# Performance work log

Measured on AMD Instinct MI355X. Metric: run time of the kernel, lower is better.

The kernel has to match this reference:

```python
import jax, jax.numpy as jnp
import numpy as np

N_NODES = 100000
N_EDGES = 1600000
D_FEAT = 128
HIDDEN = 256


def setup_inputs() -> dict:
    key = jax.random.key(0)
    k1, k2, k3, k4, k5, k6, k7 = jax.random.split(key, 7)
    h = jax.random.normal(k1, (N_NODES, D_FEAT), dtype=jnp.float32)
    src = jax.random.randint(k2, (N_EDGES,), 0, N_NODES, dtype=jnp.int64)
    dst = jax.random.randint(k3, (N_EDGES,), 0, N_NODES, dtype=jnp.int64)
    # Linear weights, torch layout: W [out, in], b [out]
    lim1 = 1.0 / np.sqrt(2 * D_FEAT)
    W1_w = jax.random.uniform(k4, (HIDDEN, 2 * D_FEAT), minval=-lim1, maxval=lim1, dtype=jnp.float32)
    W1_b = jax.random.uniform(k5, (HIDDEN,), minval=-lim1, maxval=lim1, dtype=jnp.float32)
    lim2 = 1.0 / np.sqrt(HIDDEN)
    W2_w = jax.random.uniform(k6, (1, HIDDEN), minval=-lim2, maxval=lim2, dtype=jnp.float32)
    W2_b = jax.random.uniform(k7, (1,), minval=-lim2, maxval=lim2, dtype=jnp.float32)
    return {"h": h, "src": src, "dst": dst, "W1_w": W1_w, "W1_b": W1_b, "W2_w": W2_w, "W2_b": W2_b}


def reference(h, src, dst, W1_w, W1_b, W2_w, W2_b):
    # gather per-edge src/dst node features and concat: [E, 2D]
    x = jnp.concatenate([h[src], h[dst]], axis=1)
    # Linear -> ReLU -> Linear, squeeze last dim -> [E]
    hid = jax.nn.relu(x @ W1_w.T + W1_b)          # [E, H]
    score = (hid @ W2_w.T + W2_b)[:, 0]           # [E]
    return score
```

## Files before the change

### kernel.cpp

```cpp
#include <hip/hip_runtime.h>


#define NNODES 100000
#define E_TOTAL 1600000
#define D 128
#define K2 256
#define H 256

typedef short bf16x8 __attribute__((ext_vector_type(8)));
typedef short bf16x4 __attribute__((ext_vector_type(4)));
typedef float f32x4 __attribute__((ext_vector_type(4)));
typedef const __attribute__((address_space(1))) unsigned short* gas_t;
typedef __attribute__((address_space(3))) unsigned short* las_t;

__device__ __forceinline__ unsigned short f2bf(float f) {
    unsigned u = __float_as_uint(f);
    u += 0x7fff + ((u >> 16) & 1);
    return (unsigned short)(u >> 16);
}
__device__ __forceinline__ float bf2f(unsigned short s) {
    return __uint_as_float((unsigned)s << 16);
}

__global__ void cvt_kernel(const float* __restrict__ h, const float* __restrict__ w1,
                           unsigned short* __restrict__ hbf, unsigned short* __restrict__ w1bf,
                           int n4h, int n4w) {
    int i = blockIdx.x * blockDim.x + threadIdx.x;
    const float* s; unsigned short* d; int j;
    if (i < n4h) { s = h; d = hbf; j = i; }
    else if (i < n4h + n4w) { s = w1; d = w1bf; j = i - n4h; }
    else return;
    float4 v = ((const float4*)s)[j];
    ushort4 o;
    o.x = f2bf(v.x); o.y = f2bf(v.y); o.z = f2bf(v.z); o.w = f2bf(v.w);
    ((ushort4*)d)[j] = o;
}

__global__ void cvt_w1(const float* __restrict__ W1, unsigned short* __restrict__ w1bf, int n4) {
    int i = blockIdx.x * blockDim.x + threadIdx.x;
    if (i >= n4) return;
    float4 v = ((const float4*)W1)[i];
    ushort4 o;
    o.x = f2bf(v.x); o.y = f2bf(v.y); o.z = f2bf(v.z); o.w = f2bf(v.w);
    ((ushort4*)w1bf)[i] = o;
}

__global__ __launch_bounds__(256, 2) void u_gemm2(
    const unsigned short* __restrict__ hbf,
    const unsigned short* __restrict__ w1bf,
    const float* __restrict__ b1,
    unsigned short* __restrict__ Us,
    unsigned short* __restrict__ Ud)
{
    __shared__ __align__(16) unsigned short A[64 * 128];
    __shared__ __align__(16) unsigned short S[64 * 268];

    const int tid = threadIdx.x;
    const int wave = tid >> 6;
    const int lane = tid & 63;
    const int l15 = lane & 15;
    const int quad = lane >> 4;

    const int tile = blockIdx.x >> 1;
    const int half = blockIdx.x & 1;
    const int r0 = tile * 64;
    int rows = NNODES - r0; if (rows > 64) rows = 64;
    const int koff = half * 128;
    unsigned short* U = half ? Ud : Us;

#pragma unroll
    for (int it = 0; it < 4; ++it) {
        const int s = it * 256 + tid;
        const int r = s >> 4;
        const int p = s & 15;
        const int c = p ^ (r & 15);
        if (r < rows)
            __builtin_amdgcn_global_load_lds(
                (gas_t)(hbf + (size_t)(r0 + r) * D + c * 8),
                (las_t)(A + it * 2048 + wave * 512), 16, 0, 0);
    }

    bf16x8 B[4][4];
    float bias[4];
#pragma unroll
    for (int nt = 0; nt < 4; ++nt) {
        const int n = wave * 64 + nt * 16 + l15;
        bias[nt] = half ? 0.f : b1[n];
#pragma unroll
        for (int kit = 0; kit < 4; ++kit)
            B[kit][nt] = *(const bf16x8*)(w1bf + (size_t)n * K2 + koff + kit * 32 + quad * 8);
    }

    __syncthreads();

    f32x4 acc[4][4];
    const f32x4 zero = {0.f, 0.f, 0.f, 0.f};
#pragma unroll
    for (int ms = 0; ms < 4; ++ms)
#pragma unroll
        for (int nt = 0; nt < 4; ++nt)
            acc[ms][nt] = zero;

#pragma unroll
    for (int kit = 0; kit < 4; ++kit) {
        bf16x8 a[4];
#pragma unroll
        for (int ms = 0; ms < 4; ++ms) {
            const int row = ms * 16 + l15;
            const int p = (kit * 4 + quad) ^ l15;
            a[ms] = *(const bf16x8*)&A[row * 128 + p * 8];
        }
#pragma unroll
        for (int ms = 0; ms < 4; ++ms)
#pragma unroll
            for (int nt = 0; nt < 4; ++nt)
                acc[ms][nt] = __builtin_amdgcn_mfma_f32_16x16x32_bf16(
                    a[ms], B[kit][nt], acc[ms][nt], 0, 0, 0);
    }

#pragma unroll
    for (int ms = 0; ms < 4; ++ms)
#pragma unroll
        for (int r = 0; r < 4; ++r) {
            const int m = ms * 16 + quad * 4 + r;
#pragma unroll
            for (int nt = 0; nt < 4; ++nt)
                S[m * 268 + wave * 64 + nt * 16 + l15] =
                    f2bf(acc[ms][nt][r] + bias[nt]);
        }
    __syncthreads();

#pragma unroll
    for (int i = 0; i < 8; ++i) {
        const int j = i * 256 + tid;
        const int row = j >> 5;
        const int cc = j & 31;
        if (row < rows) {
            bf16x8 vv = *(const bf16x8*)&S[row * 268 + cc * 8];
            *(bf16x8*)(U + (size_t)(r0 + row) * H + cc * 8) = vv;
        }
    }
}

__global__ __launch_bounds__(256) void edge_score(
    const unsigned short* __restrict__ Us,
    const unsigned short* __restrict__ Ud,
    const int* __restrict__ srcE,
    const int* __restrict__ dstE,
    const float* __restrict__ w2,
    const float* __restrict__ b2p,
    float* __restrict__ out,
    int grp0, int ngrp)
{
    const int gt = blockIdx.x * 256 + threadIdx.x;
    const int l = gt & 15;
    const int q = gt >> 4;
    const int Q = (gridDim.x * 256) >> 4;

    float w2v[16];
#pragma unroll
    for (int j = 0; j < 16; ++j) w2v[j] = w2[l * 16 + j];
    const float b2 = *b2p;

    for (int g = grp0 + q; g < grp0 + ngrp; g += Q) {
        const int e0 = g * 4;
        const int4 s4 = *(const int4*)(srcE + e0);
        const int4 d4 = *(const int4*)(dstE + e0);
        const int sv[4] = {s4.x, s4.y, s4.z, s4.w};
        const int dv[4] = {d4.x, d4.y, d4.z, d4.w};

        bf16x8 u[4][2], v[4][2];
#pragma unroll
        for (int k = 0; k < 4; ++k) {
            const bf16x8* us = (const bf16x8*)(Us + (size_t)sv[k] * H + l * 16);
            const bf16x8* ud = (const bf16x8*)(Ud + (size_t)dv[k] * H + l * 16);
            u[k][0] = us[0]; u[k][1] = us[1];
            v[k][0] = ud[0]; v[k][1] = ud[1];
        }

        float4 res;
        float* resp = (float*)&res;
#pragma unroll
        for (int k = 0; k < 4; ++k) {
            float acc = 0.f;
#pragma unroll
            for (int j = 0; j < 8; ++j) {
                float hv = bf2f((unsigned short)u[k][0][j]) + bf2f((unsigned short)v[k][0][j]);
                acc = fmaf(fmaxf(hv, 0.f), w2v[j], acc);
            }
#pragma unroll
            for (int j = 0; j < 8; ++j) {
                float hv = bf2f((unsigned short)u[k][1][j]) + bf2f((unsigned short)v[k][1][j]);
                acc = fmaf(fmaxf(hv, 0.f), w2v[j + 8], acc);
            }
            acc += __shfl_xor(acc, 1, 16);
            acc += __shfl_xor(acc, 2, 16);
            acc += __shfl_xor(acc, 4, 16);
            acc += __shfl_xor(acc, 8, 16);
            resp[k] = acc + b2;
        }
        if (l == 0) *(float4*)(out + e0) = res;
    }
}


#define TILE_M 32
#define NTILES (E_TOTAL / TILE_M)
#define GRID 2500

#if defined(__has_attribute)
#if __has_attribute(amdgpu_waves_per_eu)
#define LB __launch_bounds__(256) __attribute__((amdgpu_waves_per_eu(2, 2)))
#else
#define LB __launch_bounds__(256, 2)
#endif
#else
#define LB __launch_bounds__(256, 2)
#endif

__global__ LB void edge_mlp(
    const unsigned short* __restrict__ hbf,
    const int* __restrict__ srcE,
    const int* __restrict__ dstE,
    const unsigned short* __restrict__ w1bf,
    const float* __restrict__ b1,
    const float* __restrict__ w2,
    const float* __restrict__ b2p,
    float* __restrict__ out)
{
    __shared__ __align__(16) unsigned short X[2][TILE_M * K2];
    __shared__ float red[2][TILE_M][5];

    const int tid = threadIdx.x;
    const int wave = tid >> 6;
    const int lane = tid & 63;
    const int lane15 = lane & 15;
    const int quad = lane >> 4;

    bf16x8 B[8][4];
#pragma unroll
    for (int kit = 0; kit < 8; ++kit)
#pragma unroll
        for (int nt = 0; nt < 4; ++nt) {
            int n = wave * 64 + nt * 16 + lane15;
            int k = kit * 32 + quad * 8;
            B[kit][nt] = *(const bf16x8*)(w1bf + n * K2 + k);
        }

    float b1v[4], w2v[4];
#pragma unroll
    for (int nt = 0; nt < 4; ++nt) {
        int n = wave * 64 + nt * 16 + lane15;
        b1v[nt] = b1[n];
        w2v[nt] = w2[n];
    }
    const float b2 = *b2p;

    const int r_off = tid >> 5;
    const int c = (tid & 31) ^ (r_off & 7);
    const int half = c >> 4;
    const int fc = c & 15;
    const int* idx_base = half ? dstE : srcE;
    const int gshort = fc * 8;

    const int t0 = blockIdx.x;
    int inode[4];

#pragma unroll
    for (int it = 0; it < 4; ++it)
        inode[it] = idx_base[t0 * TILE_M + it * 8 + r_off];
#pragma unroll
    for (int it = 0; it < 4; ++it)
        __builtin_amdgcn_global_load_lds(
            (gas_t)(hbf + inode[it] * D + gshort),
            (las_t)(&X[0][0] + it * 2048 + wave * 512), 16, 0, 0);
    {
        const int t1 = t0 + GRID;
#pragma unroll
        for (int it = 0; it < 4; ++it)
            inode[it] = idx_base[t1 * TILE_M + it * 8 + r_off];
    }

    int buf = 0;
    int prev_eb = -1;

    for (int tile = t0; tile < NTILES; tile += GRID) {
        __syncthreads();

        const int nt1 = tile + GRID;
        if (nt1 < NTILES) {
            unsigned short* Xn = &X[buf ^ 1][0];
#pragma unroll
            for (int it = 0; it < 4; ++it)
                __builtin_amdgcn_global_load_lds(
                    (gas_t)(hbf + inode[it] * D + gshort),
                    (las_t)(Xn + it * 2048 + wave * 512), 16, 0, 0);
        }
        const int nt2 = tile + 2 * GRID;
        if (nt2 < NTILES) {
            const int eb2 = nt2 * TILE_M;
#pragma unroll
            for (int it = 0; it < 4; ++it)
                inode[it] = idx_base[eb2 + it * 8 + r_off];
        }
        if (prev_eb >= 0 && tid < TILE_M) {
            float s = b2;
#pragma unroll
            for (int w = 0; w < 4; ++w) s += red[buf ^ 1][tid][w];
            out[prev_eb + tid] = s;
        }

        const unsigned short* Xc = &X[buf][0];
        f32x4 acc[2][4];
        const f32x4 zero = {0.f, 0.f, 0.f, 0.f};
#pragma unroll
        for (int ms = 0; ms < 2; ++ms)
#pragma unroll
            for (int nt = 0; nt < 4; ++nt)
                acc[ms][nt] = zero;

#pragma unroll
        for (int kit = 0; kit < 8; ++kit) {
            const int p8 = (((kit * 4 + quad) ^ (lane15 & 7))) * 8;
            bf16x8 a[2];
#pragma unroll
            for (int ms = 0; ms < 2; ++ms)
                a[ms] = *(const bf16x8*)&Xc[(ms * 16 + lane15) * K2 + p8];
#pragma unroll
            for (int ms = 0; ms < 2; ++ms)
#pragma unroll
                for (int nt = 0; nt < 4; ++nt)
                    acc[ms][nt] = __builtin_amdgcn_mfma_f32_16x16x32_bf16(
                        a[ms], B[kit][nt], acc[ms][nt], 0, 0, 0);
        }

#pragma unroll
        for (int ms = 0; ms < 2; ++ms)
#pragma unroll
            for (int r = 0; r < 4; ++r) {
                float p = 0.f;
#pragma unroll
                for (int nt = 0; nt < 4; ++nt) {
                    float hv = acc[ms][nt][r] + b1v[nt];
                    p = fmaf(fmaxf(hv, 0.f), w2v[nt], p);
                }
                p += __shfl_xor(p, 1, 16);
                p += __shfl_xor(p, 2, 16);
                p += __shfl_xor(p, 4, 16);
                p += __shfl_xor(p, 8, 16);
                if (lane15 == 0) red[buf][ms * 16 + quad * 4 + r][wave] = p;
            }
        prev_eb = tile * TILE_M;
        buf ^= 1;
    }

    __syncthreads();
    if (prev_eb >= 0 && tid < TILE_M) {
        float s = b2;
#pragma unroll
        for (int w = 0; w < 4; ++w) s += red[buf ^ 1][tid][w];
        out[prev_eb + tid] = s;
    }
}


extern "C" void kernel_launch(void* const* d_in, const int* in_sizes, int n_in,
                              void* d_out, int out_size, void* d_ws, size_t ws_size,
                              hipStream_t stream) {
    const float* h    = (const float*)d_in[0];
    const int*   srcE = (const int*)d_in[1];
    const int*   dstE = (const int*)d_in[2];
    const float* W1   = (const float*)d_in[3];
    const float* b1   = (const float*)d_in[4];
    const float* w2   = (const float*)d_in[5];
    const float* b2   = (const float*)d_in[6];
    float* out = (float*)d_out;

    char* ws = (char*)d_ws;
    const size_t offUs   = 0;
    const size_t offUd   = 51200000;
    const size_t offHbf  = 102400000;
    const size_t offW1v2 = 128000000;
    const size_t needV2  = offW1v2 + 131072;
    const size_t offW1v1 = 102400000;
    const size_t needV1  = offW1v1 + 131072;

    const int NGRP = E_TOTAL / 4;

    if (ws_size >= needV2) {
        unsigned short* Us   = (unsigned short*)(ws + offUs);
        unsigned short* Ud   = (unsigned short*)(ws + offUd);
        unsigned short* hbf  = (unsigned short*)(ws + offHbf);
        unsigned short* w1bf = (unsigned short*)(ws + offW1v2);

        int n4h = NNODES * D / 4, n4w = H * K2 / 4;
        cvt_kernel<<<(n4h + n4w + 255) / 256, 256, 0, stream>>>(h, W1, hbf, w1bf, n4h, n4w);
        u_gemm2<<<2 * ((NNODES + 63) / 64), 256, 0, stream>>>(hbf, w1bf, b1, Us, Ud);

        const int C = NGRP / 4;
        edge_score<<<2048, 256, 0, stream>>>(Us, Ud, srcE, dstE, w2, b2, out, 0 * C, C);
        edge_score<<<2048, 256, 0, stream>>>(Us, Ud, srcE, dstE, w2, b2, out, 1 * C, C);
        edge_score<<<2048, 256, 0, stream>>>(Us, Ud, srcE, dstE, w2, b2, out, 2 * C, C);
        edge_score<<<2048, 256, 0, stream>>>(Us, Ud, srcE, dstE, w2, b2, out, 3 * C, C);
    } else if (ws_size >= needV1) {
        unsigned short* hbf  = (unsigned short*)d_ws;
        unsigned short* w1bf = hbf + (size_t)NNODES * D;
        int n4h = NNODES * D / 4, n4w = H * K2 / 4;
        cvt_kernel<<<(n4h + n4w + 255) / 256, 256, 0, stream>>>(h, W1, hbf, w1bf, n4h, n4w);
        edge_mlp<<<GRID, 256, 0, stream>>>(hbf, srcE, dstE, w1bf, b1, w2, b2, out);
    } else {
        unsigned short* hbf  = (unsigned short*)d_ws;
        unsigned short* w1bf = hbf + (size_t)NNODES * D;
        int n4h = NNODES * D / 4, n4w = H * K2 / 4;
        cvt_kernel<<<(n4h + n4w + 255) / 256, 256, 0, stream>>>(h, W1, hbf, w1bf, n4h, n4w);
        edge_mlp<<<GRID, 256, 0, stream>>>(hbf, srcE, dstE, w1bf, b1, w2, b2, out);
    }
}
```

Before: 367.9 us.

## Split node GEMM over output halves, drop LDS staging, merge edge launches

The node-level GEMM now splits each tile's 256 output columns across two blocks. This halves per-thread accumulators and B registers, and the launch bound rises to four blocks per CU. The LDS staging buffer for output is removed: each lane writes packed pairs of bf16 straight to global in an interleaved column order, and the edge kernel permutes its w2 weights to match. The four edge_score launches are merged into one larger grid, which cuts launch overhead. The trade-offs are smaller, less coalesced global stores and A tiles loaded twice.

```diff
diff --git a/kernel.cpp b/kernel.cpp
--- a/kernel.cpp
+++ b/kernel.cpp
@@ -8,7 +8,6 @@
 #define H 256
 
 typedef short bf16x8 __attribute__((ext_vector_type(8)));
-typedef short bf16x4 __attribute__((ext_vector_type(4)));
 typedef float f32x4 __attribute__((ext_vector_type(4)));
 typedef const __attribute__((address_space(1))) unsigned short* gas_t;
 typedef __attribute__((address_space(3))) unsigned short* las_t;
@@ -36,16 +35,7 @@
     ((ushort4*)d)[j] = o;
 }
 
-__global__ void cvt_w1(const float* __restrict__ W1, unsigned short* __restrict__ w1bf, int n4) {
-    int i = blockIdx.x * blockDim.x + threadIdx.x;
-    if (i >= n4) return;
-    float4 v = ((const float4*)W1)[i];
-    ushort4 o;
-    o.x = f2bf(v.x); o.y = f2bf(v.y); o.z = f2bf(v.z); o.w = f2bf(v.w);
-    ((ushort4*)w1bf)[i] = o;
-}
-
-__global__ __launch_bounds__(256, 2) void u_gemm2(
+__global__ __launch_bounds__(256, 4) void u_gemm3(
     const unsigned short* __restrict__ hbf,
     const unsigned short* __restrict__ w1bf,
     const float* __restrict__ b1,
@@ -53,7 +43,6 @@
     unsigned short* __restrict__ Ud)
 {
     __shared__ __align__(16) unsigned short A[64 * 128];
-    __shared__ __align__(16) unsigned short S[64 * 268];
 
     const int tid = threadIdx.x;
     const int wave = tid >> 6;
@@ -61,8 +50,9 @@
     const int l15 = lane & 15;
     const int quad = lane >> 4;
 
-    const int tile = blockIdx.x >> 1;
-    const int half = blockIdx.x & 1;
+    const int tile = blockIdx.x >> 2;
+    const int half = (blockIdx.x >> 1) & 1;
+    const int nh = blockIdx.x & 1;
     const int r0 = tile * 64;
     int rows = NNODES - r0; if (rows > 64) rows = 64;
     const int koff = half * 128;
@@ -80,11 +70,11 @@
                 (las_t)(A + it * 2048 + wave * 512), 16, 0, 0);
     }
 
-    bf16x8 B[4][4];
-    float bias[4];
-#pragma unroll
-    for (int nt = 0; nt < 4; ++nt) {
-        const int n = wave * 64 + nt * 16 + l15;
+    bf16x8 B[4][2];
+    float bias[2];
+#pragma unroll
+    for (int nt = 0; nt < 2; ++nt) {
+        const int n = nh * 128 + wave * 32 + nt * 16 + l15;
         bias[nt] = half ? 0.f : b1[n];
 #pragma unroll
         for (int kit = 0; kit < 4; ++kit)
@@ -93,12 +83,12 @@
 
     __syncthreads();
 
-    f32x4 acc[4][4];
+    f32x4 acc[4][2];
     const f32x4 zero = {0.f, 0.f, 0.f, 0.f};
 #pragma unroll
     for (int ms = 0; ms < 4; ++ms)
 #pragma unroll
-        for (int nt = 0; nt < 4; ++nt)
+        for (int nt = 0; nt < 2; ++nt)
             acc[ms][nt] = zero;
 
 #pragma unroll
@@ -113,31 +103,22 @@
 #pragma unroll
         for (int ms = 0; ms < 4; ++ms)
 #pragma unroll
-            for (int nt = 0; nt < 4; ++nt)
+            for (int nt = 0; nt < 2; ++nt)
                 acc[ms][nt] = __builtin_amdgcn_mfma_f32_16x16x32_bf16(
                     a[ms], B[kit][nt], acc[ms][nt], 0, 0, 0);
     }
 
-#pragma unroll
-    for (int ms = 0; ms < 4; ++ms)
+    const int coff = nh * 128 + wave * 32 + l15 * 2;
+#pragma unroll
+    for (int ms = 0; ms < 4; ++ms) {
 #pragma unroll
         for (int r = 0; r < 4; ++r) {
             const int m = ms * 16 + quad * 4 + r;
-#pragma unroll
-            for (int nt = 0; nt < 4; ++nt)
-                S[m * 268 + wave * 64 + nt * 16 + l15] =
-                    f2bf(acc[ms][nt][r] + bias[nt]);
-        }
-    __syncthreads();
-
-#pragma unroll
-    for (int i = 0; i < 8; ++i) {
-        const int j = i * 256 + tid;
-        const int row = j >> 5;
-        const int cc = j & 31;
-        if (row < rows) {
-            bf16x8 vv = *(const bf16x8*)&S[row * 268 + cc * 8];
-            *(bf16x8*)(U + (size_t)(r0 + row) * H + cc * 8) = vv;
+            if (m < rows) {
+                const unsigned lo = f2bf(acc[ms][0][r] + bias[0]);
+                const unsigned hi = f2bf(acc[ms][1][r] + bias[1]);
+                *(unsigned*)(U + (size_t)(r0 + m) * H + coff) = lo | (hi << 16);
+            }
         }
     }
 }
@@ -149,20 +130,24 @@
     const int* __restrict__ dstE,
     const float* __restrict__ w2,
     const float* __restrict__ b2p,
-    float* __restrict__ out,
-    int grp0, int ngrp)
+    float* __restrict__ out)
 {
     const int gt = blockIdx.x * 256 + threadIdx.x;
     const int l = gt & 15;
     const int q = gt >> 4;
     const int Q = (gridDim.x * 256) >> 4;
+    const int NGRP = E_TOTAL / 4;
 
     float w2v[16];
 #pragma unroll
-    for (int j = 0; j < 16; ++j) w2v[j] = w2[l * 16 + j];
+    for (int j = 0; j < 16; ++j) {
+        const int cp = l * 16 + j;
+        const int n = (cp & ~31) + ((cp & 1) << 4) + ((cp & 31) >> 1);
+        w2v[j] = w2[n];
+    }
     const float b2 = *b2p;
 
-    for (int g = grp0 + q; g < grp0 + ngrp; g += Q) {
+    for (int g = q; g < NGRP; g += Q) {
         const int e0 = g * 4;
         const int4 s4 = *(const int4*)(srcE + e0);
         const int4 d4 = *(const int4*)(dstE + e0);
@@ -380,34 +365,19 @@
     const size_t offUs   = 0;
     const size_t offUd   = 51200000;
     const size_t offHbf  = 102400000;
-    const size_t offW1v2 = 128000000;
-    const size_t needV2  = offW1v2 + 131072;
-    const size_t offW1v1 = 102400000;
-    const size_t needV1  = offW1v1 + 131072;
-
-    const int NGRP = E_TOTAL / 4;
-
-    if (ws_size >= needV2) {
+    const size_t offW1bf = 128000000;
+    const size_t need    = offW1bf + 131072;
+
+    if (ws_size >= need) {
         unsigned short* Us   = (unsigned short*)(ws + offUs);
         unsigned short* Ud   = (unsigned short*)(ws + offUd);
         unsigned short* hbf  = (unsigned short*)(ws + offHbf);
-        unsigned short* w1bf = (unsigned short*)(ws + offW1v2);
+        unsigned short* w1bf = (unsigned short*)(ws + offW1bf);
 
         int n4h = NNODES * D / 4, n4w = H * K2 / 4;
         cvt_kernel<<<(n4h + n4w + 255) / 256, 256, 0, stream>>>(h, W1, hbf, w1bf, n4h, n4w);
-        u_gemm2<<<2 * ((NNODES + 63) / 64), 256, 0, stream>>>(hbf, w1bf, b1, Us, Ud);
-
-        const int C = NGRP / 4;
-        edge_score<<<2048, 256, 0, stream>>>(Us, Ud, srcE, dstE, w2, b2, out, 0 * C, C);
-        edge_score<<<2048, 256, 0, stream>>>(Us, Ud, srcE, dstE, w2, b2, out, 1 * C, C);
-        edge_score<<<2048, 256, 0, stream>>>(Us, Ud, srcE, dstE, w2, b2, out, 2 * C, C);
-        edge_score<<<2048, 256, 0, stream>>>(Us, Ud, srcE, dstE, w2, b2, out, 3 * C, C);
-    } else if (ws_size >= needV1) {
-        unsigned short* hbf  = (unsigned short*)d_ws;
-        unsigned short* w1bf = hbf + (size_t)NNODES * D;
-        int n4h = NNODES * D / 4, n4w = H * K2 / 4;
-        cvt_kernel<<<(n4h + n4w + 255) / 256, 256, 0, stream>>>(h, W1, hbf, w1bf, n4h, n4w);
-        edge_mlp<<<GRID, 256, 0, stream>>>(hbf, srcE, dstE, w1bf, b1, w2, b2, out);
+        u_gemm3<<<4 * ((NNODES + 63) / 64), 256, 0, stream>>>(hbf, w1bf, b1, Us, Ud);
+        edge_score<<<4096, 256, 0, stream>>>(Us, Ud, srcE, dstE, w2, b2, out);
     } else {
         unsigned short* hbf  = (unsigned short*)d_ws;
         unsigned short* w1bf = hbf + (size_t)NNODES * D;
```

Result: faster. 357.5 us (-2.8%).
